# Kernel tuning notes

Measured on AMD Instinct MI355X. Metric: run time of the kernel, lower is better.

Reference implementation:

```python
import jax, jax.numpy as jnp
import numpy as np

BETA = 1.0

def setup_inputs() -> dict:
    key = jax.random.key(0)
    k1, k2 = jax.random.split(key)
    g = jax.random.normal(k1, (4, 2048, 4096), dtype=jnp.float32)
    W = jax.random.normal(k2, (4096, 16384), dtype=jnp.float32) * 0.02
    return {"g": g, "W": W}

def reference(g, W):
    # column-normalize W over the input dim n (dim=0 in torch)
    norm = jnp.linalg.norm(W, axis=0, keepdims=True)  # [1, n_hidden]
    hidsig = jnp.einsum('btn,nh->bth', g, W / norm)    # [B, T, n_hidden]
    hidlag = (1.0 / BETA) * jax.nn.logsumexp(BETA * hidsig, axis=-1)  # [B, T]
    return hidlag.reshape(-1, hidlag.shape[-1])
```

## Files before the change

### kernel.cpp

```cpp
#include <hip/hip_runtime.h>
#include <hip/hip_bf16.h>

#define M_TOTAL 8192
#define K_DIM   4096
#define H_DIM   16384

#define BM 256
#define BN 256
#define BK 64
#define NKT (K_DIM / BK)

typedef __attribute__((ext_vector_type(8))) short   short8;
typedef __attribute__((ext_vector_type(4))) float   f32x4;
typedef __attribute__((ext_vector_type(8))) unsigned short u16x8;

static __device__ __forceinline__ unsigned short f2bf(float f) {
    unsigned int x = __float_as_uint(f);
    x += 0x7fffu + ((x >> 16) & 1u);
    return (unsigned short)(x >> 16);
}

__global__ void cast_bf16_kernel(const float* __restrict__ in,
                                 unsigned short* __restrict__ out, long n) {
    long i = ((long)blockIdx.x * blockDim.x + threadIdx.x) * 8;
    if (i >= n) return;
    const float4* p = (const float4*)(in + i);
    float4 a = p[0];
    float4 b = p[1];
    u16x8 o;
    o[0] = f2bf(a.x); o[1] = f2bf(a.y); o[2] = f2bf(a.z); o[3] = f2bf(a.w);
    o[4] = f2bf(b.x); o[5] = f2bf(b.y); o[6] = f2bf(b.z); o[7] = f2bf(b.w);
    *(u16x8*)(out + i) = o;
}

__global__ void transpose_norm_kernel(const float* __restrict__ W,
                                      unsigned short* __restrict__ Wt,
                                      float* __restrict__ norm2) {
    __shared__ float tile[64][65];
    __shared__ float np[64];
    const int h0 = blockIdx.x * 64;
    const int n0 = blockIdx.y * 64;
    const int t  = threadIdx.x;
    const int c  = t & 63;
    const int r4 = t >> 6;

    if (t < 64) np[t] = 0.f;
    __syncthreads();

    float sq = 0.f;
#pragma unroll
    for (int it = 0; it < 16; ++it) {
        int r = it * 4 + r4;
        float v = W[(size_t)(n0 + r) * H_DIM + h0 + c];
        tile[r][c] = v;
        sq += v * v;
    }
    atomicAdd(&np[c], sq);
    __syncthreads();

    const int chunk = t & 7;
    const int hr    = t >> 3;
#pragma unroll
    for (int it = 0; it < 2; ++it) {
        int hrow = hr + it * 32;
        u16x8 o;
#pragma unroll
        for (int j = 0; j < 8; ++j)
            o[j] = f2bf(tile[chunk * 8 + j][hrow]);
        *(u16x8*)&Wt[(size_t)(h0 + hrow) * K_DIM + n0 + chunk * 8] = o;
    }
    if (t < 64) atomicAdd(&norm2[h0 + t], np[t]);
}

__global__ __launch_bounds__(512)
void gemm_lse_kernel(const unsigned short* __restrict__ A,
                     const unsigned short* __restrict__ Bt,
                     const float* __restrict__ norm2,
                     float* __restrict__ sums) {
    __shared__ __attribute__((aligned(16))) unsigned short As[2][BM][BK];
    __shared__ __attribute__((aligned(16))) unsigned short Bs[2][BN][BK];

    const int tid  = threadIdx.x;
    const int wave = tid >> 6;
    const int lane = tid & 63;
    const int l15  = lane & 15;
    const int quad = lane >> 4;
    const int wm   = wave >> 2;
    const int wn   = wave & 3;

    const int bid = blockIdx.x;
    const int xcd = bid & 7;
    const int li  = bid >> 3;
    const int m0  = ((xcd & 1) * 16 + (li & 15)) * BM;
    const int h0  = ((xcd >> 1) * 16 + (li >> 4)) * BN;

    const int ri = lane >> 3;
    const int sc = ((lane & 7) ^ ri) * 8;
    const unsigned short* ag = A  + (size_t)(m0 + wave * 8 + ri) * K_DIM + sc;
    const unsigned short* bg = Bt + (size_t)(h0 + wave * 8 + ri) * K_DIM + sc;

#define STAGE_A(BF_, BASE_, KT_)                                               \
    __builtin_amdgcn_global_load_lds(                                          \
        (const __attribute__((address_space(1))) void*)                        \
            (ag + (size_t)(BASE_) * K_DIM + (KT_) * BK),                       \
        (__attribute__((address_space(3))) void*)&As[BF_][(BASE_) + wave * 8][0], \
        16, 0, 0)
#define STAGE_B(BF_, BASE_, KT_)                                               \
    __builtin_amdgcn_global_load_lds(                                          \
        (const __attribute__((address_space(1))) void*)                        \
            (bg + (size_t)(BASE_) * K_DIM + (KT_) * BK),                       \
        (__attribute__((address_space(3))) void*)&Bs[BF_][(BASE_) + wave * 8][0], \
        16, 0, 0)

    const int arow = wm * 128 + l15;
    const int brow = wn * 64 + l15;
    const int sl0  = ((quad)     ^ (l15 & 7)) * 8;
    const int sl1  = ((4 + quad) ^ (l15 & 7)) * 8;

#define LDA(D_, BF_, FM_, KS_) D_ = *(const short8*)&As[BF_][arow + (FM_) * 16][(KS_) ? sl1 : sl0]
#define LDB(D_, BF_, FN_, KS_) D_ = *(const short8*)&Bs[BF_][brow + (FN_) * 16][(KS_) ? sl1 : sl0]
#define MFMA(A_, B_, C_) C_ = __builtin_amdgcn_mfma_f32_16x16x32_bf16(A_, B_, C_, 0, 0, 0)

    f32x4 acc[8][4];
#pragma unroll
    for (int i = 0; i < 8; ++i)
#pragma unroll
        for (int j = 0; j < 4; ++j)
            acc[i][j] = (f32x4){0.f, 0.f, 0.f, 0.f};

    STAGE_A(0, 0, 0);   STAGE_A(0, 128, 0);
    STAGE_A(0, 64, 0);  STAGE_A(0, 192, 0);
    STAGE_B(0, 0, 0);   STAGE_B(0, 64, 0);
    STAGE_B(0, 128, 0); STAGE_B(0, 192, 0);
    STAGE_A(1, 0, 1);   STAGE_A(1, 128, 1);
    asm volatile("s_waitcnt vmcnt(2)" ::: "memory");
    __builtin_amdgcn_s_barrier();

    short8 b[4][2];
    short8 a00, a01, a10, a11;

#define PHASE_MFMA(Q_)                                                         \
    __builtin_amdgcn_s_barrier();                                              \
    __builtin_amdgcn_s_setprio(1);                                             \
    _Pragma("unroll")                                                          \
    for (int fn = 0; fn < 4; ++fn) {                                           \
        MFMA(a00, b[fn][0], acc[2 * (Q_)][fn]);                                \
        MFMA(a01, b[fn][1], acc[2 * (Q_)][fn]);                                \
        MFMA(a10, b[fn][0], acc[2 * (Q_) + 1][fn]);                            \
        MFMA(a11, b[fn][1], acc[2 * (Q_) + 1][fn]);                            \
    }                                                                          \
    __builtin_amdgcn_s_setprio(0)

#pragma unroll 2
    for (int t = 0; t < NKT; ++t) {
        const int buf  = t & 1;
        const int nbuf = buf ^ 1;

        LDA(a00, buf, 0, 0); LDA(a01, buf, 0, 1);
        LDA(a10, buf, 1, 0); LDA(a11, buf, 1, 1);
#pragma unroll
        for (int fn = 0; fn < 4; ++fn) {
            LDB(b[fn][0], buf, fn, 0);
            LDB(b[fn][1], buf, fn, 1);
        }
        if (t < NKT - 1) { STAGE_A(nbuf, 64, t + 1); STAGE_A(nbuf, 192, t + 1); }
        PHASE_MFMA(0);
        __builtin_amdgcn_s_barrier();

        LDA(a00, buf, 2, 0); LDA(a01, buf, 2, 1);
        LDA(a10, buf, 3, 0); LDA(a11, buf, 3, 1);
        if (t < NKT - 1) {
            STAGE_B(nbuf, 0, t + 1);   STAGE_B(nbuf, 64, t + 1);
            STAGE_B(nbuf, 128, t + 1); STAGE_B(nbuf, 192, t + 1);
        }
        PHASE_MFMA(1);
        __builtin_amdgcn_s_barrier();

        LDA(a00, buf, 4, 0); LDA(a01, buf, 4, 1);
        LDA(a10, buf, 5, 0); LDA(a11, buf, 5, 1);
        if (t < NKT - 2) { STAGE_A(buf, 0, t + 2); STAGE_A(buf, 128, t + 2); }
        PHASE_MFMA(2);
        __builtin_amdgcn_s_barrier();

        LDA(a00, buf, 6, 0); LDA(a01, buf, 6, 1);
        LDA(a10, buf, 7, 0); LDA(a11, buf, 7, 1);
        PHASE_MFMA(3);

        if (t < NKT - 2) {
            asm volatile("s_waitcnt vmcnt(2)" ::: "memory");
            __builtin_amdgcn_s_barrier();
        } else if (t == NKT - 2) {
            asm volatile("s_waitcnt vmcnt(0)" ::: "memory");
            __builtin_amdgcn_s_barrier();
        }
    }

    float rn[4];
#pragma unroll
    for (int fn = 0; fn < 4; ++fn)
        rn[fn] = rsqrtf(norm2[h0 + wn * 64 + fn * 16 + l15]);

#pragma unroll
    for (int fm = 0; fm < 8; ++fm) {
#pragma unroll
        for (int r2 = 0; r2 < 4; ++r2) {
            float s = 0.f;
#pragma unroll
            for (int fn = 0; fn < 4; ++fn)
                s += __expf(acc[fm][fn][r2] * rn[fn]);
            s += __shfl_xor(s, 1);
            s += __shfl_xor(s, 2);
            s += __shfl_xor(s, 4);
            s += __shfl_xor(s, 8);
            if (l15 == 0)
                atomicAdd(&sums[m0 + wm * 128 + fm * 16 + quad * 4 + r2], s);
        }
    }
#undef STAGE_A
#undef STAGE_B
#undef LDA
#undef LDB
#undef MFMA
#undef PHASE_MFMA
}

__global__ void finalize_kernel(const float* __restrict__ sums,
                                float* __restrict__ out, int n) {
    int i = blockIdx.x * blockDim.x + threadIdx.x;
    if (i < n) out[i] = logf(sums[i]);
}

extern "C" void kernel_launch(void* const* d_in, const int* in_sizes, int n_in,
                              void* d_out, int out_size, void* d_ws, size_t ws_size,
                              hipStream_t stream) {
    const float* g = (const float*)d_in[0];
    const float* W = (const float*)d_in[1];
    float* out = (float*)d_out;

    char* ws = (char*)d_ws;
    unsigned short* gbf   = (unsigned short*)ws;
    unsigned short* wt    = (unsigned short*)(ws + (size_t)67108864);
    float*          norm2 = (float*)(ws + (size_t)67108864 + 134217728);
    float*          sums  = (float*)(ws + (size_t)67108864 + 134217728 + 65536);

    hipMemsetAsync(norm2, 0, (H_DIM + M_TOTAL) * sizeof(float), stream);

    cast_bf16_kernel<<<(M_TOTAL * (long)K_DIM) / (256 * 8), 256, 0, stream>>>(
        g, gbf, (long)M_TOTAL * K_DIM);

    transpose_norm_kernel<<<dim3(H_DIM / 64, K_DIM / 64), 256, 0, stream>>>(
        W, wt, norm2);

    gemm_lse_kernel<<<(H_DIM / BN) * (M_TOTAL / BM), 512, 0, stream>>>(
        gbf, wt, norm2, sums);

    finalize_kernel<<<(M_TOTAL + 255) / 256, 256, 0, stream>>>(sums, out, M_TOTAL);
}
```

Measured before the change: 1.465 ms.

## Restructure GEMM main loop into 8-wave ping-pong clusters with deeper prefetch

Result: faster. 1.352 ms (-7.7%).

```diff
diff --git a/kernel.cpp b/kernel.cpp
--- a/kernel.cpp
+++ b/kernel.cpp
@@ -72,7 +72,7 @@
     if (t < 64) atomicAdd(&norm2[h0 + t], np[t]);
 }
 
-__global__ __launch_bounds__(512)
+__global__ __launch_bounds__(512, 2)
 void gemm_lse_kernel(const unsigned short* __restrict__ A,
                      const unsigned short* __restrict__ Bt,
                      const float* __restrict__ norm2,
@@ -119,7 +119,6 @@
 
 #define LDA(D_, BF_, FM_, KS_) D_ = *(const short8*)&As[BF_][arow + (FM_) * 16][(KS_) ? sl1 : sl0]
 #define LDB(D_, BF_, FN_, KS_) D_ = *(const short8*)&Bs[BF_][brow + (FN_) * 16][(KS_) ? sl1 : sl0]
-#define MFMA(A_, B_, C_) C_ = __builtin_amdgcn_mfma_f32_16x16x32_bf16(A_, B_, C_, 0, 0, 0)
 
     f32x4 acc[8][4];
 #pragma unroll
@@ -127,72 +126,70 @@
 #pragma unroll
         for (int j = 0; j < 4; ++j)
             acc[i][j] = (f32x4){0.f, 0.f, 0.f, 0.f};
+
+    short8 sa0[4], sb0[4], sa1[4], sb1[4];
+
+#define CLUSTER(FB_, SA_, SB_)                                                 \
+    __builtin_amdgcn_s_barrier();                                              \
+    __builtin_amdgcn_s_setprio(1);                                             \
+    _Pragma("unroll")                                                          \
+    for (int fm = 0; fm < 4; ++fm)                                             \
+        _Pragma("unroll")                                                      \
+        for (int fn = 0; fn < 4; ++fn)                                         \
+            acc[(FB_) + fm][fn] = __builtin_amdgcn_mfma_f32_16x16x32_bf16(     \
+                SA_[fm], SB_[fn], acc[(FB_) + fm][fn], 0, 0, 0);               \
+    __builtin_amdgcn_s_setprio(0);                                             \
+    __builtin_amdgcn_s_barrier()
 
     STAGE_A(0, 0, 0);   STAGE_A(0, 128, 0);
     STAGE_A(0, 64, 0);  STAGE_A(0, 192, 0);
     STAGE_B(0, 0, 0);   STAGE_B(0, 64, 0);
     STAGE_B(0, 128, 0); STAGE_B(0, 192, 0);
     STAGE_A(1, 0, 1);   STAGE_A(1, 128, 1);
-    asm volatile("s_waitcnt vmcnt(2)" ::: "memory");
+    STAGE_B(1, 0, 1);   STAGE_B(1, 64, 1);
+    STAGE_B(1, 128, 1); STAGE_B(1, 192, 1);
+    asm volatile("s_waitcnt vmcnt(6)" ::: "memory");
     __builtin_amdgcn_s_barrier();
 
-    short8 b[4][2];
-    short8 a00, a01, a10, a11;
-
-#define PHASE_MFMA(Q_)                                                         \
-    __builtin_amdgcn_s_barrier();                                              \
-    __builtin_amdgcn_s_setprio(1);                                             \
-    _Pragma("unroll")                                                          \
-    for (int fn = 0; fn < 4; ++fn) {                                           \
-        MFMA(a00, b[fn][0], acc[2 * (Q_)][fn]);                                \
-        MFMA(a01, b[fn][1], acc[2 * (Q_)][fn]);                                \
-        MFMA(a10, b[fn][0], acc[2 * (Q_) + 1][fn]);                            \
-        MFMA(a11, b[fn][1], acc[2 * (Q_) + 1][fn]);                            \
-    }                                                                          \
-    __builtin_amdgcn_s_setprio(0)
+    LDA(sa0[0], 0, 0, 0); LDA(sa0[1], 0, 1, 0);
+    LDA(sa0[2], 0, 2, 0); LDA(sa0[3], 0, 3, 0);
+    LDB(sb0[0], 0, 0, 0); LDB(sb0[1], 0, 1, 0);
+    LDB(sb0[2], 0, 2, 0); LDB(sb0[3], 0, 3, 0);
 
 #pragma unroll 2
     for (int t = 0; t < NKT; ++t) {
         const int buf  = t & 1;
         const int nbuf = buf ^ 1;
 
-        LDA(a00, buf, 0, 0); LDA(a01, buf, 0, 1);
-        LDA(a10, buf, 1, 0); LDA(a11, buf, 1, 1);
-#pragma unroll
-        for (int fn = 0; fn < 4; ++fn) {
-            LDB(b[fn][0], buf, fn, 0);
-            LDB(b[fn][1], buf, fn, 1);
+        LDA(sa1[0], buf, 0, 1); LDA(sa1[1], buf, 1, 1);
+        LDA(sa1[2], buf, 2, 1); LDA(sa1[3], buf, 3, 1);
+        LDB(sb1[0], buf, 0, 1); LDB(sb1[1], buf, 1, 1);
+        LDB(sb1[2], buf, 2, 1); LDB(sb1[3], buf, 3, 1);
+        if (t < NKT - 1) { STAGE_A(nbuf, 64, t + 1); STAGE_A(nbuf, 192, t + 1); }
+        asm volatile("s_waitcnt vmcnt(8)" ::: "memory");
+        CLUSTER(0, sa0, sb0);
+
+        LDA(sa0[0], buf, 4, 0); LDA(sa0[1], buf, 5, 0);
+        LDA(sa0[2], buf, 6, 0); LDA(sa0[3], buf, 7, 0);
+        CLUSTER(0, sa1, sb1);
+
+        LDA(sa1[0], buf, 4, 1); LDA(sa1[1], buf, 5, 1);
+        LDA(sa1[2], buf, 6, 1); LDA(sa1[3], buf, 7, 1);
+        if (t < NKT - 2) { STAGE_A(buf, 0, t + 2); STAGE_A(buf, 128, t + 2); }
+        asm volatile("s_waitcnt vmcnt(4)" ::: "memory");
+        CLUSTER(4, sa0, sb0);
+
+        if (t < NKT - 1) {
+            LDA(sa0[0], nbuf, 0, 0); LDA(sa0[1], nbuf, 1, 0);
+            LDA(sa0[2], nbuf, 2, 0); LDA(sa0[3], nbuf, 3, 0);
+            LDB(sb0[0], nbuf, 0, 0); LDB(sb0[1], nbuf, 1, 0);
+            LDB(sb0[2], nbuf, 2, 0); LDB(sb0[3], nbuf, 3, 0);
         }
-        if (t < NKT - 1) { STAGE_A(nbuf, 64, t + 1); STAGE_A(nbuf, 192, t + 1); }
-        PHASE_MFMA(0);
-        __builtin_amdgcn_s_barrier();
-
-        LDA(a00, buf, 2, 0); LDA(a01, buf, 2, 1);
-        LDA(a10, buf, 3, 0); LDA(a11, buf, 3, 1);
-        if (t < NKT - 1) {
-            STAGE_B(nbuf, 0, t + 1);   STAGE_B(nbuf, 64, t + 1);
-            STAGE_B(nbuf, 128, t + 1); STAGE_B(nbuf, 192, t + 1);
+        if (t < NKT - 2) {
+            STAGE_B(buf, 0, t + 2);   STAGE_B(buf, 64, t + 2);
+            STAGE_B(buf, 128, t + 2); STAGE_B(buf, 192, t + 2);
         }
-        PHASE_MFMA(1);
-        __builtin_amdgcn_s_barrier();
-
-        LDA(a00, buf, 4, 0); LDA(a01, buf, 4, 1);
-        LDA(a10, buf, 5, 0); LDA(a11, buf, 5, 1);
-        if (t < NKT - 2) { STAGE_A(buf, 0, t + 2); STAGE_A(buf, 128, t + 2); }
-        PHASE_MFMA(2);
-        __builtin_amdgcn_s_barrier();
-
-        LDA(a00, buf, 6, 0); LDA(a01, buf, 6, 1);
-        LDA(a10, buf, 7, 0); LDA(a11, buf, 7, 1);
-        PHASE_MFMA(3);
-
-        if (t < NKT - 2) {
-            asm volatile("s_waitcnt vmcnt(2)" ::: "memory");
-            __builtin_amdgcn_s_barrier();
-        } else if (t == NKT - 2) {
-            asm volatile("s_waitcnt vmcnt(0)" ::: "memory");
-            __builtin_amdgcn_s_barrier();
-        }
+        CLUSTER(4, sa1, sb1);
     }
 
     float rn[4];
@@ -220,8 +217,7 @@
 #undef STAGE_B
 #undef LDA
 #undef LDB
-#undef MFMA
-#undef PHASE_MFMA
+#undef CLUSTER
 }
 
 __global__ void finalize_kernel(const float* __restrict__ sums,
```
